# Kernel tuning notes

Measured on AMD Instinct MI355X. Metric: run time of the kernel, lower is better.

The kernel has to match this reference:

```python
import jax, jax.numpy as jnp
import numpy as np

B, D, S = 8192, 32, 8
M = 2 ** S - 1  # 255 combinatorial masks


def _mask_gen():
    # rows are binary expansions of 1..2^S-1, exactly as mask_gen in the module
    m = np.array([[int(c) for c in bin(v)[2:].zfill(S)] for v in range(1, 2 ** S)],
                 dtype=np.float32)
    return jnp.asarray(m)  # [M, S]


def setup_inputs() -> dict:
    key = jax.random.key(0)
    kx, kb, klw = jax.random.split(key, 3)
    x = jax.random.normal(kx, (B, 1, S), dtype=jnp.float32)
    k = jnp.ones((D, S), dtype=jnp.float32) * 10.0
    buf = jax.random.uniform(kb, (D, S), dtype=jnp.float32) - 0.5
    w = buf * 2.0
    q = buf * 1.0
    mask = _mask_gen()
    lin_w = jax.random.normal(klw, (1, M), dtype=jnp.float32) / np.sqrt(M)
    lin_b = jnp.zeros((1,), dtype=jnp.float32)
    return {"x": x, "k": k, "w": w, "q": q, "mask": mask,
            "lin_w": lin_w, "lin_b": lin_b}


def reference(x, k, w, q, mask, lin_w, lin_b):
    # synapse gate: sigmoid in (0,1), so log is safe
    s = jax.nn.sigmoid(k * (w * x - q))          # [B, D, S]
    # prod_s (s ** mask) == exp(mask @ log s), fused broadcast pow + prod-reduce
    out = jnp.exp(jnp.einsum("bds,ms->bdm", jnp.log(s), mask))  # [B, D, M]
    out = out @ lin_w.T + lin_b                   # [B, D, 1]
    return out[..., 0][:, None, :]                # [B, 1, D]
```

## Files before the change

### kernel.cpp

```cpp
#include <hip/hip_runtime.h>
#include <math.h>


#define BLOCK 256

__global__ __launch_bounds__(BLOCK) void dendrite_kernel(
    const float* __restrict__ x,
    const float* __restrict__ k,
    const float* __restrict__ w,
    const float* __restrict__ q,
    const float* __restrict__ lin_w,
    const float* __restrict__ lin_b,
    float* __restrict__ out)
{
    __shared__ float s_t[256];

    const int tid = threadIdx.x;
    s_t[tid] = (tid == 0) ? 0.0f : lin_w[tid - 1];
    __syncthreads();

    const int gid = blockIdx.x * BLOCK + tid;
    const int b = gid >> 5;
    const int d = gid & 31;

    const float4* xv = (const float4*)(x + (size_t)b * 8);
    const float4 xa = xv[0], xb = xv[1];
    const float4* kv = (const float4*)(k + d * 8);
    const float4 ka = kv[0], kb = kv[1];
    const float4* wv = (const float4*)(w + d * 8);
    const float4 wa = wv[0], wb = wv[1];
    const float4* qv = (const float4*)(q + d * 8);
    const float4 qa = qv[0], qb = qv[1];

    const float xx[8] = {xa.x, xa.y, xa.z, xa.w, xb.x, xb.y, xb.z, xb.w};
    const float kk[8] = {ka.x, ka.y, ka.z, ka.w, kb.x, kb.y, kb.z, kb.w};
    const float ww[8] = {wa.x, wa.y, wa.z, wa.w, wb.x, wb.y, wb.z, wb.w};
    const float qq[8] = {qa.x, qa.y, qa.z, qa.w, qb.x, qb.y, qb.z, qb.w};

    float s[8];
#pragma unroll
    for (int j = 0; j < 8; ++j) {
        const float z = kk[j] * fmaf(ww[j], xx[j], -qq[j]);
        const float e = __expf(-z);
        s[j] = __builtin_amdgcn_rcpf(1.0f + e);
    }

    float Phi[16], Plo[16];
    Phi[0] = 1.0f; Plo[0] = 1.0f;
#pragma unroll
    for (int v = 1; v < 16; ++v) {
        const int lb  = v & (-v);
        const int idx = (lb == 1) ? 0 : (lb == 2) ? 1 : (lb == 4) ? 2 : 3;
        Phi[v] = Phi[v ^ lb] * s[3 - idx];
        Plo[v] = Plo[v ^ lb] * s[7 - idx];
    }

    float acc = 0.0f;
#pragma unroll
    for (int h = 0; h < 16; ++h) {
        const float4* row = (const float4*)(s_t + (h << 4));
        const float4 r0 = row[0], r1 = row[1], r2 = row[2], r3 = row[3];
        float inner;
        inner = r0.x * Plo[0];
        inner = fmaf(r0.y, Plo[1],  inner);
        inner = fmaf(r0.z, Plo[2],  inner);
        inner = fmaf(r0.w, Plo[3],  inner);
        inner = fmaf(r1.x, Plo[4],  inner);
        inner = fmaf(r1.y, Plo[5],  inner);
        inner = fmaf(r1.z, Plo[6],  inner);
        inner = fmaf(r1.w, Plo[7],  inner);
        inner = fmaf(r2.x, Plo[8],  inner);
        inner = fmaf(r2.y, Plo[9],  inner);
        inner = fmaf(r2.z, Plo[10], inner);
        inner = fmaf(r2.w, Plo[11], inner);
        inner = fmaf(r3.x, Plo[12], inner);
        inner = fmaf(r3.y, Plo[13], inner);
        inner = fmaf(r3.z, Plo[14], inner);
        inner = fmaf(r3.w, Plo[15], inner);
        acc = fmaf(Phi[h], inner, acc);
    }
    out[gid] = acc + lin_b[0];
}

extern "C" void kernel_launch(void* const* d_in, const int* in_sizes, int n_in,
                              void* d_out, int out_size, void* d_ws, size_t ws_size,
                              hipStream_t stream) {
    const float* x     = (const float*)d_in[0];
    const float* k     = (const float*)d_in[1];
    const float* w     = (const float*)d_in[2];
    const float* q     = (const float*)d_in[3];
    const float* lin_w = (const float*)d_in[5];
    const float* lin_b = (const float*)d_in[6];
    float* out = (float*)d_out;

    const int total = out_size;
    const int grid  = total / BLOCK;
    dendrite_kernel<<<grid, BLOCK, 0, stream>>>(x, k, w, q, lin_w, lin_b, out);
}
```

Baseline: 68.08 us.

## Compute two outputs per thread with packed float2 FMA and interleaved weight table

```diff
diff --git a/kernel.cpp b/kernel.cpp
--- a/kernel.cpp
+++ b/kernel.cpp
@@ -2,9 +2,12 @@
 #include <math.h>
 
 
+typedef float v2f __attribute__((ext_vector_type(2)));
+
 #define BLOCK 256
+#define OUTS_PER_BLOCK 512
 
-__global__ __launch_bounds__(BLOCK) void dendrite_kernel(
+__global__ __launch_bounds__(BLOCK, 2) void dendrite_kernel(
     const float* __restrict__ x,
     const float* __restrict__ k,
     const float* __restrict__ w,
@@ -13,18 +16,27 @@
     const float* __restrict__ lin_b,
     float* __restrict__ out)
 {
-    __shared__ float s_t[256];
+    __shared__ float s_t2[256];
 
     const int tid = threadIdx.x;
-    s_t[tid] = (tid == 0) ? 0.0f : lin_w[tid - 1];
+    {
+        const float tv = (tid == 0) ? 0.0f : lin_w[tid - 1];
+        const int p = tid >> 5;
+        const int e = (tid >> 4) & 1;
+        const int l = tid & 15;
+        s_t2[(p << 5) + (l << 1) + e] = tv;
+    }
     __syncthreads();
 
-    const int gid = blockIdx.x * BLOCK + tid;
-    const int b = gid >> 5;
-    const int d = gid & 31;
+    const int gid0 = blockIdx.x * OUTS_PER_BLOCK + tid;
+    const int gid1 = gid0 + BLOCK;
+    const int b0 = gid0 >> 5;
+    const int d  = gid0 & 31;
 
-    const float4* xv = (const float4*)(x + (size_t)b * 8);
-    const float4 xa = xv[0], xb = xv[1];
+    const float4* xv0 = (const float4*)(x + (size_t)b0 * 8);
+    const float4 xa0 = xv0[0], xb0 = xv0[1];
+    const float4* xv1 = (const float4*)(x + (size_t)(b0 + 8) * 8);
+    const float4 xa1 = xv1[0], xb1 = xv1[1];
     const float4* kv = (const float4*)(k + d * 8);
     const float4 ka = kv[0], kb = kv[1];
     const float4* wv = (const float4*)(w + d * 8);
@@ -32,54 +44,71 @@
     const float4* qv = (const float4*)(q + d * 8);
     const float4 qa = qv[0], qb = qv[1];
 
-    const float xx[8] = {xa.x, xa.y, xa.z, xa.w, xb.x, xb.y, xb.z, xb.w};
-    const float kk[8] = {ka.x, ka.y, ka.z, ka.w, kb.x, kb.y, kb.z, kb.w};
-    const float ww[8] = {wa.x, wa.y, wa.z, wa.w, wb.x, wb.y, wb.z, wb.w};
-    const float qq[8] = {qa.x, qa.y, qa.z, qa.w, qb.x, qb.y, qb.z, qb.w};
+    const float xx0[8] = {xa0.x, xa0.y, xa0.z, xa0.w, xb0.x, xb0.y, xb0.z, xb0.w};
+    const float xx1[8] = {xa1.x, xa1.y, xa1.z, xa1.w, xb1.x, xb1.y, xb1.z, xb1.w};
+    const float kk[8]  = {ka.x, ka.y, ka.z, ka.w, kb.x, kb.y, kb.z, kb.w};
+    const float ww[8]  = {wa.x, wa.y, wa.z, wa.w, wb.x, wb.y, wb.z, wb.w};
+    const float qq[8]  = {qa.x, qa.y, qa.z, qa.w, qb.x, qb.y, qb.z, qb.w};
 
-    float s[8];
+    float s0v[8], s1v[8];
 #pragma unroll
     for (int j = 0; j < 8; ++j) {
-        const float z = kk[j] * fmaf(ww[j], xx[j], -qq[j]);
-        const float e = __expf(-z);
-        s[j] = __builtin_amdgcn_rcpf(1.0f + e);
+        const float z0 = kk[j] * fmaf(ww[j], xx0[j], -qq[j]);
+        const float z1 = kk[j] * fmaf(ww[j], xx1[j], -qq[j]);
+        s0v[j] = __builtin_amdgcn_rcpf(1.0f + __expf(-z0));
+        s1v[j] = __builtin_amdgcn_rcpf(1.0f + __expf(-z1));
     }
 
-    float Phi[16], Plo[16];
-    Phi[0] = 1.0f; Plo[0] = 1.0f;
+    float Phi0[16], Phi1[16];
+    v2f   Plo0[16], Plo1[16];
+    Phi0[0] = 1.0f; Phi1[0] = 1.0f;
+    Plo0[0] = (v2f){1.0f, 1.0f};
+    Plo1[0] = (v2f){1.0f, 1.0f};
 #pragma unroll
     for (int v = 1; v < 16; ++v) {
         const int lb  = v & (-v);
         const int idx = (lb == 1) ? 0 : (lb == 2) ? 1 : (lb == 4) ? 2 : 3;
-        Phi[v] = Phi[v ^ lb] * s[3 - idx];
-        Plo[v] = Plo[v ^ lb] * s[7 - idx];
+        Phi0[v] = Phi0[v ^ lb] * s0v[3 - idx];
+        Phi1[v] = Phi1[v ^ lb] * s1v[3 - idx];
+        Plo0[v] = Plo0[v ^ lb] * s0v[7 - idx];
+        Plo1[v] = Plo1[v ^ lb] * s1v[7 - idx];
     }
 
-    float acc = 0.0f;
+    v2f phi0p[8], phi1p[8];
 #pragma unroll
-    for (int h = 0; h < 16; ++h) {
-        const float4* row = (const float4*)(s_t + (h << 4));
+    for (int p = 0; p < 8; ++p) {
+        phi0p[p] = (v2f){Phi0[2 * p], Phi0[2 * p + 1]};
+        phi1p[p] = (v2f){Phi1[2 * p], Phi1[2 * p + 1]};
+    }
+
+    v2f acc0 = {0.0f, 0.0f};
+    v2f acc1 = {0.0f, 0.0f};
+#pragma unroll
+    for (int p = 0; p < 8; ++p) {
+        const float4* row = (const float4*)(s_t2 + (p << 5));
         const float4 r0 = row[0], r1 = row[1], r2 = row[2], r3 = row[3];
-        float inner;
-        inner = r0.x * Plo[0];
-        inner = fmaf(r0.y, Plo[1],  inner);
-        inner = fmaf(r0.z, Plo[2],  inner);
-        inner = fmaf(r0.w, Plo[3],  inner);
-        inner = fmaf(r1.x, Plo[4],  inner);
-        inner = fmaf(r1.y, Plo[5],  inner);
-        inner = fmaf(r1.z, Plo[6],  inner);
-        inner = fmaf(r1.w, Plo[7],  inner);
-        inner = fmaf(r2.x, Plo[8],  inner);
-        inner = fmaf(r2.y, Plo[9],  inner);
-        inner = fmaf(r2.z, Plo[10], inner);
-        inner = fmaf(r2.w, Plo[11], inner);
-        inner = fmaf(r3.x, Plo[12], inner);
-        inner = fmaf(r3.y, Plo[13], inner);
-        inner = fmaf(r3.z, Plo[14], inner);
-        inner = fmaf(r3.w, Plo[15], inner);
-        acc = fmaf(Phi[h], inner, acc);
+        const float4 r4 = row[4], r5 = row[5], r6 = row[6], r7 = row[7];
+        const v2f pr[16] = {
+            {r0.x, r0.y}, {r0.z, r0.w}, {r1.x, r1.y}, {r1.z, r1.w},
+            {r2.x, r2.y}, {r2.z, r2.w}, {r3.x, r3.y}, {r3.z, r3.w},
+            {r4.x, r4.y}, {r4.z, r4.w}, {r5.x, r5.y}, {r5.z, r5.w},
+            {r6.x, r6.y}, {r6.z, r6.w}, {r7.x, r7.y}, {r7.z, r7.w}};
+        v2f i0a = {0.0f, 0.0f}, i0b = {0.0f, 0.0f};
+        v2f i1a = {0.0f, 0.0f}, i1b = {0.0f, 0.0f};
+#pragma unroll
+        for (int l = 0; l < 8; ++l) {
+            i0a += pr[l] * Plo0[l];
+            i1a += pr[l] * Plo1[l];
+            i0b += pr[l + 8] * Plo0[l + 8];
+            i1b += pr[l + 8] * Plo1[l + 8];
+        }
+        acc0 += phi0p[p] * (i0a + i0b);
+        acc1 += phi1p[p] * (i1a + i1b);
     }
-    out[gid] = acc + lin_b[0];
+
+    const float bias = lin_b[0];
+    out[gid0] = acc0.x + acc0.y + bias;
+    out[gid1] = acc1.x + acc1.y + bias;
 }
 
 extern "C" void kernel_launch(void* const* d_in, const int* in_sizes, int n_in,
@@ -94,6 +123,6 @@
     float* out = (float*)d_out;
 
     const int total = out_size;
-    const int grid  = total / BLOCK;
+    const int grid  = total / OUTS_PER_BLOCK;
     dendrite_kernel<<<grid, BLOCK, 0, stream>>>(x, k, w, q, lin_w, lin_b, out);
 }
```

Result: no change. 69.17 us (+1.6%).
